# Kernel tuning notes

Hardware: AMD Instinct MI355X
Metric: run time of the kernel (lower is better)

The kernel has to match this reference:

```python
import jax, jax.numpy as jnp
import numpy as np

EMBED_DIM = 1024
HEAD_SIZE = 64
N_HEAD = 16
N_QUERY_GROUPS = 4
SEQ_LEN = 2048
BATCH = 8


def setup_inputs() -> dict:
    key = jax.random.key(0)
    ks = jax.random.split(key, 7)
    s = 1.0 / np.sqrt(EMBED_DIM)
    x = jax.random.normal(ks[0], (BATCH, SEQ_LEN, EMBED_DIM), dtype=jnp.float32)
    Wq = jax.random.uniform(ks[1], (EMBED_DIM, N_HEAD * HEAD_SIZE), jnp.float32, -s, s)
    bq = jax.random.uniform(ks[2], (N_HEAD * HEAD_SIZE,), jnp.float32, -s, s)
    Wk = jax.random.uniform(ks[3], (EMBED_DIM, N_QUERY_GROUPS * HEAD_SIZE), jnp.float32, -s, s)
    bk = jax.random.uniform(ks[4], (N_QUERY_GROUPS * HEAD_SIZE,), jnp.float32, -s, s)
    Wv = jax.random.uniform(ks[5], (EMBED_DIM, N_QUERY_GROUPS * HEAD_SIZE), jnp.float32, -s, s)
    bv = jax.random.uniform(ks[6], (N_QUERY_GROUPS * HEAD_SIZE,), jnp.float32, -s, s)
    return {"x": x, "Wq": Wq, "bq": bq, "Wk": Wk, "bk": bk, "Wv": Wv, "bv": bv}


def reference(x, Wq, bq, Wk, bk, Wv, bv):
    B, T, _ = x.shape
    rep = N_HEAD // N_QUERY_GROUPS  # queries per group
    Q = x @ Wq + bq  # (B, T, H*hs)
    # GQA: torch .repeat tiles the group-block [g0..g3, g0..g3, ...]
    K = (x @ Wk + bk).reshape(B, T, N_QUERY_GROUPS, HEAD_SIZE)
    K = jnp.tile(K, (1, 1, rep, 1)).reshape(B, T, N_HEAD * HEAD_SIZE)
    V = (x @ Wv + bv).reshape(B, T, N_QUERY_GROUPS, HEAD_SIZE)
    V = jnp.tile(V, (1, 1, rep, 1)).reshape(B, T, N_HEAD * HEAD_SIZE)
    # flattened-head scores: contract over full H*hs dim (as in source)
    att = jnp.einsum('btd,bsd->bts', Q, K)  # (B, T, T)
    causal = jnp.triu(jnp.ones((T, T), dtype=bool), k=1)
    mask = jnp.where(causal, jnp.float32(-jnp.inf), jnp.float32(0.0))[None, None]  # (1,1,T,T)
    att = att + mask  # broadcasts to (1, B, T, T), matching torch semantics
    att = jax.nn.softmax(att, axis=-1) / jnp.sqrt(jnp.float32(HEAD_SIZE))  # post-hoc scale, as in source
    out = jnp.einsum('xbts,bsd->xbtd', att, V)  # (1, B, T, H*hs)
    return out
```

## Files before the change

### kernel.cpp

```cpp
#include <hip/hip_runtime.h>
#include <float.h>
#include <stdint.h>

#define T_ 2048
#define DG 256

typedef _Float16 half8 __attribute__((ext_vector_type(8)));
typedef _Float16 half4v __attribute__((ext_vector_type(4)));
typedef __fp16 fp16x2 __attribute__((ext_vector_type(2)));
typedef float f32x4 __attribute__((ext_vector_type(4)));
typedef float f32x16 __attribute__((ext_vector_type(16)));

__device__ __forceinline__ void gload16(const void* g, void* l) {
  __builtin_amdgcn_global_load_lds(
      (const __attribute__((address_space(1))) unsigned int*)g,
      (__attribute__((address_space(3))) unsigned int*)l, 16, 0, 0);
}
#define WAIT_VM0()   do { asm volatile("s_waitcnt vmcnt(0)" ::: "memory"); __builtin_amdgcn_sched_barrier(0); } while (0)
#define WAIT_LGKM0() do { asm volatile("s_waitcnt lgkmcnt(0)" ::: "memory"); __builtin_amdgcn_sched_barrier(0); } while (0)

__global__ __launch_bounds__(256) void prep_w(
    const float* __restrict__ Wq, const float* __restrict__ bq,
    const float* __restrict__ Wk, const float* __restrict__ bk,
    const float* __restrict__ Wv, const float* __restrict__ bv,
    _Float16* __restrict__ Wt, float* __restrict__ bcat) {
  int idx = blockIdx.x * 256 + threadIdx.x;
  int n = idx >> 10, k = idx & 1023;
  float v;
  if (n < 256)      v = Wq[k * 1024 + n] + Wq[k * 1024 + n + 256]
                      + Wq[k * 1024 + n + 512] + Wq[k * 1024 + n + 768];
  else if (n < 512) v = Wk[k * 256 + n - 256];
  else              v = Wv[k * 256 + n - 512];
  Wt[idx] = (_Float16)v;
  if (k == 0) {
    float bb;
    if (n < 256)      bb = bq[n] + bq[n + 256] + bq[n + 512] + bq[n + 768];
    else if (n < 512) bb = bk[n - 256];
    else              bb = bv[n - 512];
    bcat[n] = bb;
  }
}

__global__ __launch_bounds__(256) void qkv_gemm(
    const float* __restrict__ x, const _Float16* __restrict__ Wt,
    const float* __restrict__ bcat,
    _Float16* __restrict__ Qh, _Float16* __restrict__ Kh, _Float16* __restrict__ Vt) {
  __shared__ __align__(16) uint8_t smem[49152];
  const int tid = threadIdx.x;
  const int w = tid >> 6, l = tid & 63;
  const int wr = w >> 1, wc = w & 1;
  const int lr = l & 15, lk = l >> 4;
  const int m0 = blockIdx.x * 128, n0 = blockIdx.y * 128;

  f32x4 acc[4][4] = {};

  auto stage = [&](int k0, int buf) {
    uint8_t* Ab = smem + buf * 24576;
    uint8_t* Bb = Ab + 16384;
#pragma unroll
    for (int i = 0; i < 4; ++i) {
      int si = i * 256 + tid;
      int row = si >> 3, p = si & 7;
      gload16(x + (size_t)(m0 + row) * 1024 + k0 + ((p ^ (row & 7)) << 2), Ab + si * 16);
    }
#pragma unroll
    for (int i = 0; i < 2; ++i) {
      int si = i * 256 + tid;
      int row = si >> 2, p = si & 3;
      gload16(Wt + (size_t)(n0 + row) * 1024 + k0 + ((p ^ (row & 3)) << 3), Bb + si * 16);
    }
  };

  stage(0, 0);
  __syncthreads();

  for (int kt = 0; kt < 32; ++kt) {
    int cur = kt & 1;
    if (kt < 31) stage((kt + 1) * 32, cur ^ 1);
    const uint8_t* Ab = smem + cur * 24576;
    const uint8_t* Bb = Ab + 16384;
    half8 af[4], bf[4];
#pragma unroll
    for (int mi = 0; mi < 4; ++mi) {
      int row = wr * 64 + mi * 16 + lr;
      const float* pa = (const float*)(Ab + row * 128);
      f32x4 a0 = *(const f32x4*)(pa + ((((lk << 1))     ^ (row & 7)) << 2));
      f32x4 a1 = *(const f32x4*)(pa + ((((lk << 1) | 1) ^ (row & 7)) << 2));
      half8 h;
#pragma unroll
      for (int j = 0; j < 4; ++j) { h[j] = (_Float16)a0[j]; h[j + 4] = (_Float16)a1[j]; }
      af[mi] = h;
    }
#pragma unroll
    for (int ni = 0; ni < 4; ++ni) {
      int row = wc * 64 + ni * 16 + lr;
      bf[ni] = *(const half8*)(Bb + row * 64 + ((lk ^ (row & 3)) << 4));
    }
#pragma unroll
    for (int mi = 0; mi < 4; ++mi)
#pragma unroll
      for (int ni = 0; ni < 4; ++ni)
        acc[mi][ni] = __builtin_amdgcn_mfma_f32_16x16x32_f16(af[mi], bf[ni], acc[mi][ni], 0, 0, 0);
    __syncthreads();
  }

#pragma unroll
  for (int mi = 0; mi < 4; ++mi) {
#pragma unroll
    for (int ni = 0; ni < 4; ++ni) {
      int ng = n0 + wc * 64 + ni * 16 + lr;
      int mg = m0 + wr * 64 + mi * 16 + lk * 4;
      float bias = bcat[ng];
      if (ng < 256) {
#pragma unroll
        for (int r = 0; r < 4; ++r)
          Qh[(size_t)(mg + r) * DG + ng] = (_Float16)((acc[mi][ni][r] + bias) * 1.44269504f);
      } else if (ng < 512) {
#pragma unroll
        for (int r = 0; r < 4; ++r)
          Kh[(size_t)(mg + r) * DG + (ng - 256)] = (_Float16)(acc[mi][ni][r] + bias);
      } else {
        half4v h;
#pragma unroll
        for (int r = 0; r < 4; ++r) h[r] = (_Float16)(acc[mi][ni][r] + bias);
        *(half4v*)(Vt + ((size_t)((mg >> 11) * DG + (ng - 512))) * T_ + (mg & 2047)) = h;
      }
    }
  }
}

__global__ __launch_bounds__(128, 1) void attn_mfma(
    const _Float16* __restrict__ Qg, const _Float16* __restrict__ Kg,
    const _Float16* __restrict__ Vtg, float* __restrict__ out) {
  __shared__ __align__(16) uint8_t smem[65536];
  const int tid = threadIdx.x;
  const int wv = tid >> 6;
  const int l  = tid & 63;
  const int g  = l >> 5;
  const int ln = l & 31;
  const int bid = blockIdx.x;
  const int b   = bid & 7;
  const int tile = (bid < 256) ? (63 - (bid >> 3)) : ((bid - 256) >> 3);
  const int q0 = tile * 32;

  const _Float16* Kb = Kg  + (size_t)b * T_ * DG;
  const _Float16* Vb = Vtg + (size_t)b * DG * T_;

  const _Float16* Qrow = Qg + ((size_t)(b * T_ + q0 + ln)) * DG + 8 * g;
  half8 qf[16];
#pragma unroll
  for (int kk = 0; kk < 16; ++kk) qf[kk] = *(const half8*)(Qrow + kk * 16);

  f32x16 o[8] = {};
  float m_r = -1e30f, l_r = 0.0f;

  uint8_t* myK = smem + wv * 32768;
  auto stageK = [&](int s0, int buf) {
    uint8_t* Kl = myK + buf * 16384;
#pragma unroll
    for (int i = 0; i < 16; ++i) {
      int slot = i * 64 + l;
      int row = slot >> 5, part = slot & 31;
      gload16(Kb + (size_t)(s0 + row) * DG + ((part ^ (row & 7)) << 3), Kl + i * 1024);
    }
  };

  int cur = 0;
  if (wv <= tile) stageK(wv * 32, 0);

  for (int kt = wv; kt <= tile; kt += 2) {
    WAIT_VM0();
    int s0 = kt * 32;
    half8 vf0[8], vf1[8];
#pragma unroll
    for (int dt = 0; dt < 8; ++dt) {
      const _Float16* vr = Vb + (size_t)(dt * 32 + ln) * T_ + s0 + 8 * g;
      vf0[dt] = *(const half8*)vr;
      vf1[dt] = *(const half8*)(vr + 16);
    }
    if (kt + 2 <= tile) stageK((kt + 2) * 32, cur ^ 1);
    uint8_t* Klds = myK + cur * 16384;

    f32x16 sa = {}, sb = {};
    const int xr = (ln & 7) << 4;
#pragma unroll
    for (int kk = 0; kk < 16; kk += 2) {
      half8 ka = *(const half8*)(Klds + ln * 512 + ((kk * 32 + 16 * g) ^ xr));
      half8 kb = *(const half8*)(Klds + ln * 512 + (((kk + 1) * 32 + 16 * g) ^ xr));
      sa = __builtin_amdgcn_mfma_f32_32x32x16_f16(ka, qf[kk],     sa, 0, 0, 0);
      sb = __builtin_amdgcn_mfma_f32_32x32x16_f16(kb, qf[kk + 1], sb, 0, 0, 0);
    }
    float s[16];
#pragma unroll
    for (int r = 0; r < 16; ++r) s[r] = sa[r] + sb[r];
    if (kt == tile) {
#pragma unroll
      for (int r = 0; r < 16; ++r) {
        int srow = (r & 3) + 8 * (r >> 2) + 4 * g;
        if (srow > ln) s[r] = -1e30f;
      }
    }
    float pmax = s[0];
#pragma unroll
    for (int r = 1; r < 16; ++r) pmax = fmaxf(pmax, s[r]);
    pmax = fmaxf(pmax, __shfl_xor(pmax, 32));
    if (!__all(pmax <= m_r + 8.0f)) {
      float mnew = fmaxf(m_r, pmax);
      float sc = exp2f(m_r - mnew);
      l_r *= sc;
#pragma unroll
      for (int dt = 0; dt < 8; ++dt)
#pragma unroll
        for (int r = 0; r < 16; ++r) o[dt][r] *= sc;
      m_r = mnew;
    }
    float p[16]; float psum = 0.0f;
#pragma unroll
    for (int r = 0; r < 16; ++r) { p[r] = exp2f(s[r] - m_r); psum += p[r]; }
    l_r += psum + __shfl_xor(psum, 32);

    unsigned ph[8], xh[8];
#pragma unroll
    for (int i = 0; i < 8; ++i) {
      fp16x2 t2 = __builtin_amdgcn_cvt_pkrtz(p[2 * i], p[2 * i + 1]);
      ph[i] = __builtin_bit_cast(unsigned, t2);
      xh[i] = (unsigned)__shfl_xor((int)ph[i], 32);
    }
    union U { unsigned u[4]; half8 h; };
    U f0, f1;
    f0.u[0] = g ? xh[2] : ph[0]; f0.u[1] = g ? xh[3] : ph[1];
    f0.u[2] = g ? ph[2] : xh[0]; f0.u[3] = g ? ph[3] : xh[1];
    f1.u[0] = g ? xh[6] : ph[4]; f1.u[1] = g ? xh[7] : ph[5];
    f1.u[2] = g ? ph[6] : xh[4]; f1.u[3] = g ? ph[7] : xh[5];

#pragma unroll
    for (int dt = 0; dt < 8; ++dt)
      o[dt] = __builtin_amdgcn_mfma_f32_32x32x16_f16(vf0[dt], f0.h, o[dt], 0, 0, 0);
#pragma unroll
    for (int dt = 0; dt < 8; ++dt)
      o[dt] = __builtin_amdgcn_mfma_f32_32x32x16_f16(vf1[dt], f1.h, o[dt], 0, 0, 0);
    cur ^= 1;
  }

  __syncthreads();
  if (wv == 1) {
    float* dst = (float*)(smem + 32768);
#pragma unroll
    for (int dt = 0; dt < 8; ++dt)
#pragma unroll
      for (int r = 0; r < 16; ++r)
        dst[(dt * 16 + r) * 64 + l] = o[dt][r];
    ((float*)smem)[l]      = m_r;
    ((float*)smem)[64 + l] = l_r;
  }
  __syncthreads();
  if (wv == 0) {
    float m1 = ((float*)smem)[l];
    float l1 = ((float*)smem)[64 + l];
    float M   = fmaxf(m_r, m1);
    float sc0 = exp2f(m_r - M);
    float sc1 = exp2f(m1 - M);
    float lt  = l_r * sc0 + l1 * sc1;
    float inv = 1.0f / (lt * 8.0f);
    const float* src = (const float*)(smem + 32768);
    float* chunk = (float*)(smem + 4096);
    float* ob = out + ((size_t)(b * T_ + q0)) * 1024;
#pragma unroll
    for (int dt = 0; dt < 8; ++dt) {
      WAIT_LGKM0();
#pragma unroll
      for (int r = 0; r < 16; ++r) {
        int dl = (r & 3) + 8 * (r >> 2) + 4 * g;
        float merged = (o[dt][r] * sc0 + src[(dt * 16 + r) * 64 + l] * sc1) * inv;
        chunk[ln * 33 + dl] = merged;
      }
      WAIT_LGKM0();
#pragma unroll
      for (int rr = 0; rr < 2; ++rr) {
        int qq = (l >> 2) + 16 * rr;
        int cp = (l & 3) * 8;
        float vv[8];
#pragma unroll
        for (int jj = 0; jj < 8; ++jj) vv[jj] = chunk[qq * 33 + cp + jj];
        float4 w0 = make_float4(vv[0], vv[1], vv[2], vv[3]);
        float4 w1 = make_float4(vv[4], vv[5], vv[6], vv[7]);
        float* orow = ob + (size_t)qq * 1024 + dt * 32 + cp;
#pragma unroll
        for (int rep = 0; rep < 4; ++rep) {
          *(float4*)(orow + rep * 256)     = w0;
          *(float4*)(orow + rep * 256 + 4) = w1;
        }
      }
    }
  }
}

extern "C" void kernel_launch(void* const* d_in, const int* in_sizes, int n_in,
                              void* d_out, int out_size, void* d_ws, size_t ws_size,
                              hipStream_t stream) {
  const float* x  = (const float*)d_in[0];
  const float* Wq = (const float*)d_in[1];
  const float* bq = (const float*)d_in[2];
  const float* Wk = (const float*)d_in[3];
  const float* bk = (const float*)d_in[4];
  const float* Wv = (const float*)d_in[5];
  const float* bv = (const float*)d_in[6];
  float* out = (float*)d_out;
  char* ws = (char*)d_ws;
  _Float16* Wt   = (_Float16*)ws;
  float*    bcat = (float*)(ws + 0x180000);
  _Float16* Qh   = (_Float16*)(ws + 0x181000);
  _Float16* Kh   = Qh + (size_t)16384 * 256;
  _Float16* Vt   = Kh + (size_t)16384 * 256;

  prep_w<<<3072, 256, 0, stream>>>(Wq, bq, Wk, bk, Wv, bv, Wt, bcat);
  qkv_gemm<<<dim3(128, 6), 256, 0, stream>>>(x, Wt, bcat, Qh, Kh, Vt);
  attn_mfma<<<512, 128, 0, stream>>>(Qh, Kh, Vt, out);
}
```

Measured before the change: 157.7 us.

## Overlap K prefetch with partial vmcnt wait, defer V loads, use permlane32 swaps

Issues the next K tile's LDS prefetch before waiting, then waits with a partial vmcnt so the current tile's loads complete while the new ones stay in flight. V fragment global loads move after the QK MFMAs so their latency overlaps the softmax. Cross-half shuffles become permlane32_swap instead of ds_bpermute-based shfl_xor, exp2f becomes the raw hardware exp2, and s_setprio is raised around the MFMA blocks. This risks ordering mistakes between the vmcnt counts and the V loads, and slightly different exp precision.

Result: faster. 136.5 us (-13.4%).

```diff
diff --git a/kernel.cpp b/kernel.cpp
--- a/kernel.cpp
+++ b/kernel.cpp
@@ -10,14 +10,21 @@
 typedef __fp16 fp16x2 __attribute__((ext_vector_type(2)));
 typedef float f32x4 __attribute__((ext_vector_type(4)));
 typedef float f32x16 __attribute__((ext_vector_type(16)));
+typedef unsigned uint2v __attribute__((ext_vector_type(2)));
 
 __device__ __forceinline__ void gload16(const void* g, void* l) {
   __builtin_amdgcn_global_load_lds(
       (const __attribute__((address_space(1))) unsigned int*)g,
       (__attribute__((address_space(3))) unsigned int*)l, 16, 0, 0);
 }
-#define WAIT_VM0()   do { asm volatile("s_waitcnt vmcnt(0)" ::: "memory"); __builtin_amdgcn_sched_barrier(0); } while (0)
+#define WAIT_VMC(N)  do { asm volatile("s_waitcnt vmcnt(" #N ")" ::: "memory"); __builtin_amdgcn_sched_barrier(0); } while (0)
 #define WAIT_LGKM0() do { asm volatile("s_waitcnt lgkmcnt(0)" ::: "memory"); __builtin_amdgcn_sched_barrier(0); } while (0)
+
+__device__ __forceinline__ float cross32(float x, int g) {
+  unsigned u = __builtin_bit_cast(unsigned, x);
+  uint2v r = __builtin_amdgcn_permlane32_swap(u, u, false, false);
+  return __builtin_bit_cast(float, g ? r[0] : r[1]);
+}
 
 __global__ __launch_bounds__(256) void prep_w(
     const float* __restrict__ Wq, const float* __restrict__ bq,
@@ -169,20 +176,14 @@
   if (wv <= tile) stageK(wv * 32, 0);
 
   for (int kt = wv; kt <= tile; kt += 2) {
-    WAIT_VM0();
+    if (kt + 2 <= tile) { stageK((kt + 2) * 32, cur ^ 1); WAIT_VMC(16); }
+    else                { WAIT_VMC(0); }
     int s0 = kt * 32;
-    half8 vf0[8], vf1[8];
-#pragma unroll
-    for (int dt = 0; dt < 8; ++dt) {
-      const _Float16* vr = Vb + (size_t)(dt * 32 + ln) * T_ + s0 + 8 * g;
-      vf0[dt] = *(const half8*)vr;
-      vf1[dt] = *(const half8*)(vr + 16);
-    }
-    if (kt + 2 <= tile) stageK((kt + 2) * 32, cur ^ 1);
     uint8_t* Klds = myK + cur * 16384;
 
     f32x16 sa = {}, sb = {};
     const int xr = (ln & 7) << 4;
+    __builtin_amdgcn_s_setprio(1);
 #pragma unroll
     for (int kk = 0; kk < 16; kk += 2) {
       half8 ka = *(const half8*)(Klds + ln * 512 + ((kk * 32 + 16 * g) ^ xr));
@@ -190,6 +191,16 @@
       sa = __builtin_amdgcn_mfma_f32_32x32x16_f16(ka, qf[kk],     sa, 0, 0, 0);
       sb = __builtin_amdgcn_mfma_f32_32x32x16_f16(kb, qf[kk + 1], sb, 0, 0, 0);
     }
+    __builtin_amdgcn_s_setprio(0);
+
+    half8 vf0[8], vf1[8];
+#pragma unroll
+    for (int dt = 0; dt < 8; ++dt) {
+      const _Float16* vr = Vb + (size_t)(dt * 32 + ln) * T_ + s0 + 8 * g;
+      vf0[dt] = *(const half8*)vr;
+      vf1[dt] = *(const half8*)(vr + 16);
+    }
+
     float s[16];
 #pragma unroll
     for (int r = 0; r < 16; ++r) s[r] = sa[r] + sb[r];
@@ -203,10 +214,10 @@
     float pmax = s[0];
 #pragma unroll
     for (int r = 1; r < 16; ++r) pmax = fmaxf(pmax, s[r]);
-    pmax = fmaxf(pmax, __shfl_xor(pmax, 32));
+    pmax = fmaxf(pmax, cross32(pmax, g));
     if (!__all(pmax <= m_r + 8.0f)) {
       float mnew = fmaxf(m_r, pmax);
-      float sc = exp2f(m_r - mnew);
+      float sc = __builtin_amdgcn_exp2f(m_r - mnew);
       l_r *= sc;
 #pragma unroll
       for (int dt = 0; dt < 8; ++dt)
@@ -216,29 +227,36 @@
     }
     float p[16]; float psum = 0.0f;
 #pragma unroll
-    for (int r = 0; r < 16; ++r) { p[r] = exp2f(s[r] - m_r); psum += p[r]; }
-    l_r += psum + __shfl_xor(psum, 32);
-
-    unsigned ph[8], xh[8];
+    for (int r = 0; r < 16; ++r) { p[r] = __builtin_amdgcn_exp2f(s[r] - m_r); psum += p[r]; }
+    l_r += psum + cross32(psum, g);
+
+    unsigned ph[8];
 #pragma unroll
     for (int i = 0; i < 8; ++i) {
       fp16x2 t2 = __builtin_amdgcn_cvt_pkrtz(p[2 * i], p[2 * i + 1]);
       ph[i] = __builtin_bit_cast(unsigned, t2);
-      xh[i] = (unsigned)__shfl_xor((int)ph[i], 32);
     }
     union U { unsigned u[4]; half8 h; };
     U f0, f1;
-    f0.u[0] = g ? xh[2] : ph[0]; f0.u[1] = g ? xh[3] : ph[1];
-    f0.u[2] = g ? ph[2] : xh[0]; f0.u[3] = g ? ph[3] : xh[1];
-    f1.u[0] = g ? xh[6] : ph[4]; f1.u[1] = g ? xh[7] : ph[5];
-    f1.u[2] = g ? ph[6] : xh[4]; f1.u[3] = g ? ph[7] : xh[5];
-
+    {
+      uint2v r02 = __builtin_amdgcn_permlane32_swap(ph[0], ph[2], false, false);
+      uint2v r13 = __builtin_amdgcn_permlane32_swap(ph[1], ph[3], false, false);
+      uint2v r46 = __builtin_amdgcn_permlane32_swap(ph[4], ph[6], false, false);
+      uint2v r57 = __builtin_amdgcn_permlane32_swap(ph[5], ph[7], false, false);
+      f0.u[0] = r02[0]; f0.u[2] = r02[1];
+      f0.u[1] = r13[0]; f0.u[3] = r13[1];
+      f1.u[0] = r46[0]; f1.u[2] = r46[1];
+      f1.u[1] = r57[0]; f1.u[3] = r57[1];
+    }
+
+    __builtin_amdgcn_s_setprio(1);
 #pragma unroll
     for (int dt = 0; dt < 8; ++dt)
       o[dt] = __builtin_amdgcn_mfma_f32_32x32x16_f16(vf0[dt], f0.h, o[dt], 0, 0, 0);
 #pragma unroll
     for (int dt = 0; dt < 8; ++dt)
       o[dt] = __builtin_amdgcn_mfma_f32_32x32x16_f16(vf1[dt], f1.h, o[dt], 0, 0, 0);
+    __builtin_amdgcn_s_setprio(0);
     cur ^= 1;
   }
 
@@ -258,8 +276,8 @@
     float m1 = ((float*)smem)[l];
     float l1 = ((float*)smem)[64 + l];
     float M   = fmaxf(m_r, m1);
-    float sc0 = exp2f(m_r - M);
-    float sc1 = exp2f(m1 - M);
+    float sc0 = __builtin_amdgcn_exp2f(m_r - M);
+    float sc1 = __builtin_amdgcn_exp2f(m1 - M);
     float lt  = l_r * sc0 + l1 * sc1;
     float inv = 1.0f / (lt * 8.0f);
     const float* src = (const float*)(smem + 32768);
```
